# Performance work log

Hardware: AMD Instinct MI355X
Metric: run time of the kernel (lower is better)

Reference implementation:

```python
import jax, jax.numpy as jnp
import numpy as np

ALPHA = 0.5    # SpikeAct surrogate width (act_fun(alpha=0.5))
DECAY = 0.2    # membrane decay
THRESH = 0.5   # firing threshold (requires_grad=False -> constant)


@jax.custom_vjp
def spike_act(x):
    # Heaviside spike with rectangular surrogate gradient
    return (x > 0).astype(x.dtype)

def _sa_fwd(x):
    return spike_act(x), x

def _sa_bwd(x, g):
    return (g * (jnp.abs(x) < ALPHA).astype(g.dtype),)

spike_act.defvjp(_sa_fwd, _sa_bwd)


@jax.custom_vjp
def ei_act(x):
    # EI sign gate with straight-through gradient
    return jnp.sign(x)

def _ei_fwd(x):
    return ei_act(x), None

def _ei_bwd(_, g):
    return (g,)

ei_act.defvjp(_ei_fwd, _ei_bwd)


def conv2d(x, w, b):
    # x: [B,C,H,W], w: [O,I,kh,kw] (OIHW), SAME padding, stride 1
    y = jax.lax.conv_general_dilated(
        x, w, window_strides=(1, 1), padding='SAME',
        dimension_numbers=('NCHW', 'OIHW', 'NCHW'))
    return y + b[None, :, None, None]


def setup_inputs() -> dict:
    key = jax.random.key(0)
    k0, k1, k2 = jax.random.split(key, 3)
    T, B, C, H, W, K = 8, 16, 128, 32, 32, 5
    fan_in = C * K * K
    x = jax.random.normal(k0, (T, B, C, H, W), jnp.float32)
    back_w = jax.random.normal(k1, (C, C, K, K), jnp.float32) / np.float32(np.sqrt(fan_in))
    back_b = jnp.zeros((C,), jnp.float32)
    ei_w = jax.random.normal(k2, (C, C, K, K), jnp.float32) / np.float32(np.sqrt(fan_in))
    ei_b = jnp.zeros((C,), jnp.float32)
    return {"x": x, "back_w": back_w, "back_b": back_b, "ei_w": ei_w, "ei_b": ei_b}


def reference(x, back_w, back_b, ei_w, ei_b):
    # x: [T,B,C,H,W] -> spikes over time [T,B,C,H,W]
    state_shape = x.shape[1:]
    mem0 = jnp.zeros(state_shape, x.dtype)
    spike0 = jnp.zeros(state_shape, x.dtype)

    def step(carry, xt):
        mem, spike = carry
        # integral: decayed mem + feedback-conv sigmoid gate * input
        mem = DECAY * mem + jax.nn.sigmoid(conv2d(spike, back_w, back_b)) * xt
        # calc_spike (if_ei=True path)
        ei_gate = ei_act(conv2d(mem, ei_w, ei_b))
        s = spike_act(mem - THRESH)
        mem = mem * (1.0 - s)
        spike = ei_gate * s
        return (mem, spike), spike

    _, spikes = jax.lax.scan(step, (mem0, spike0), x)
    return spikes
```

## Files before the change

### kernel.cpp

```cpp
#include <hip/hip_runtime.h>
#include <math.h>

#define TDIM 512
#define CCH  128
#define HW   32
#define OCT  4
#define ICT  2
#define NPH  16
#define SW   36
#define TROWS 12
#define PLANE (TROWS * SW)

template<int EPI>
__global__ __launch_bounds__(TDIM, 8) void lif_conv(
    const float* __restrict__ cin,
    const float* __restrict__ wgt,
    const float* __restrict__ bias,
    const float* __restrict__ aux0,
    const float* __restrict__ aux1,
    float* __restrict__ out0,
    float* __restrict__ out1,
    int first)
{
    const int ocg  = blockIdx.x;
    const int half = blockIdx.y;
    const int b    = blockIdx.z;
    const int oc0  = ocg * OCT;
    const int tid  = threadIdx.x;
    const int w    = tid >> 6;
    const int lane = tid & 63;
    const int ks   = w >> 1;
    const int rg   = w & 1;
    const int r0   = half * 16 + rg * 8;
    const int rl   = lane >> 3;
    const int cl   = (lane & 7) * 4;

    const int sks = __builtin_amdgcn_readfirstlane(ks);

    __shared__ __align__(16) float s_in[8 * ICT * PLANE];
    float* tin = s_in + w * (ICT * PLANE);

    float acc[OCT][4];
#pragma unroll
    for (int oc = 0; oc < OCT; ++oc)
#pragma unroll
        for (int j = 0; j < 4; ++j) acc[oc][j] = 0.f;

    if (!(EPI == 0 && first)) {
        const int icbase = ks * 32;
        const int sicb   = sks * 32;
        for (int i = lane; i < ICT * PLANE; i += 64) tin[i] = 0.f;

        for (int ph = 0; ph < NPH; ++ph) {
#pragma unroll
            for (int i = 0; i < 3; ++i) {
                int idx  = i * 64 + lane;
                int p    = (idx >= 96) ? 1 : 0;
                int rem  = idx - p * 96;
                int srow = rem >> 3;
                int sg   = rem & 7;
                int gr   = r0 + srow - 2;
                if ((unsigned)gr < 32u) {
                    float4 v = *(const float4*)&cin[(((size_t)b * CCH + icbase + ph * ICT + p) * HW + gr) * HW + sg * 4];
                    float* dst = &tin[p * PLANE + srow * SW + 2 + sg * 4];
                    *(float2*)dst       = make_float2(v.x, v.y);
                    *(float2*)(dst + 2) = make_float2(v.z, v.w);
                }
            }
#pragma unroll
            for (int ici = 0; ici < ICT; ++ici) {
                float win5[5][8];
#pragma unroll
                for (int kh = 0; kh < 5; ++kh) {
                    const float* src = &tin[ici * PLANE + (rl + kh) * SW + cl];
                    float4 a = *(const float4*)src;
                    float4 c = *(const float4*)(src + 4);
                    win5[kh][0] = a.x; win5[kh][1] = a.y; win5[kh][2] = a.z; win5[kh][3] = a.w;
                    win5[kh][4] = c.x; win5[kh][5] = c.y; win5[kh][6] = c.z; win5[kh][7] = c.w;
                }
                const float* wb = wgt + ((size_t)oc0 * CCH + sicb + ph * ICT + ici) * 25;
#pragma unroll
                for (int oc = 0; oc < OCT; ++oc) {
                    const float* wo = wb + oc * (CCH * 25);
#pragma unroll
                    for (int kh = 0; kh < 5; ++kh) {
#pragma unroll
                        for (int kw = 0; kw < 5; ++kw) {
                            float wv = wo[kh * 5 + kw];
                            acc[oc][0] += win5[kh][kw]     * wv;
                            acc[oc][1] += win5[kh][kw + 1] * wv;
                            acc[oc][2] += win5[kh][kw + 2] * wv;
                            acc[oc][3] += win5[kh][kw + 3] * wv;
                        }
                    }
                }
            }
        }

        __syncthreads();
        float* red = s_in;
        if (ks > 0) {
            const int slot = ((ks - 1) * 128 + rg * 64 + lane) * 17;
#pragma unroll
            for (int oc = 0; oc < OCT; ++oc)
#pragma unroll
                for (int j = 0; j < 4; ++j)
                    red[slot + oc * 4 + j] = acc[oc][j];
        }
        __syncthreads();
        if (ks == 0) {
#pragma unroll
            for (int q = 0; q < 3; ++q) {
                const int slot = (q * 128 + rg * 64 + lane) * 17;
#pragma unroll
                for (int oc = 0; oc < OCT; ++oc)
#pragma unroll
                    for (int j = 0; j < 4; ++j)
                        acc[oc][j] += red[slot + oc * 4 + j];
            }
        }
    }

    if (ks == 0) {
#pragma unroll
        for (int oc = 0; oc < OCT; ++oc) {
            const size_t pidx = (((size_t)b * CCH + oc0 + oc) * HW + (r0 + rl)) * HW + cl;
            const float bia = bias[oc0 + oc];
            float y[4];
#pragma unroll
            for (int j = 0; j < 4; ++j) y[j] = acc[oc][j] + bia;
            if (EPI == 0) {
                float4 xv = *(const float4*)(aux1 + pidx);
                float4 mv;
                if (first) { mv.x = mv.y = mv.z = mv.w = 0.f; }
                else       mv = *(const float4*)(aux0 + pidx);
                float4 mp;
                mp.x = 0.2f * mv.x + (1.f / (1.f + expf(-y[0]))) * xv.x;
                mp.y = 0.2f * mv.y + (1.f / (1.f + expf(-y[1]))) * xv.y;
                mp.z = 0.2f * mv.z + (1.f / (1.f + expf(-y[2]))) * xv.z;
                mp.w = 0.2f * mv.w + (1.f / (1.f + expf(-y[3]))) * xv.w;
                *(float4*)(out0 + pidx) = mp;
            } else {
                float4 m4 = *(const float4*)(aux0 + pidx);
                float g[4] = {
                    (y[0] > 0.f) ? 1.f : ((y[0] < 0.f) ? -1.f : 0.f),
                    (y[1] > 0.f) ? 1.f : ((y[1] < 0.f) ? -1.f : 0.f),
                    (y[2] > 0.f) ? 1.f : ((y[2] < 0.f) ? -1.f : 0.f),
                    (y[3] > 0.f) ? 1.f : ((y[3] < 0.f) ? -1.f : 0.f)};
                float m[4] = {m4.x, m4.y, m4.z, m4.w};
                float4 mn, sp;
                float s0 = (m[0] > 0.5f) ? 1.f : 0.f;
                float s1 = (m[1] > 0.5f) ? 1.f : 0.f;
                float s2 = (m[2] > 0.5f) ? 1.f : 0.f;
                float s3 = (m[3] > 0.5f) ? 1.f : 0.f;
                mn.x = m[0] * (1.f - s0); sp.x = g[0] * s0;
                mn.y = m[1] * (1.f - s1); sp.y = g[1] * s1;
                mn.z = m[2] * (1.f - s2); sp.z = g[2] * s2;
                mn.w = m[3] * (1.f - s3); sp.w = g[3] * s3;
                *(float4*)(out0 + pidx) = mn;
                *(float4*)(out1 + pidx) = sp;
            }
        }
    }
}

extern "C" void kernel_launch(void* const* d_in, const int* in_sizes, int n_in,
                              void* d_out, int out_size, void* d_ws, size_t ws_size,
                              hipStream_t stream) {
    const float* x      = (const float*)d_in[0];
    const float* back_w = (const float*)d_in[1];
    const float* back_b = (const float*)d_in[2];
    const float* ei_w   = (const float*)d_in[3];
    const float* ei_b   = (const float*)d_in[4];
    float* out = (float*)d_out;

    const size_t N = (size_t)16 * CCH * HW * HW;
    float* mem_cur  = (float*)d_ws;
    float* mem_post = mem_cur + N;

    dim3 grid(CCH / OCT, 2, 16);

    for (int t = 0; t < 8; ++t) {
        const float* spike_prev = (t == 0) ? x : (out + (size_t)(t - 1) * N);
        lif_conv<0><<<grid, TDIM, 0, stream>>>(
            spike_prev, back_w, back_b,
            mem_cur, x + (size_t)t * N,
            mem_post, nullptr, (t == 0) ? 1 : 0);
        lif_conv<1><<<grid, TDIM, 0, stream>>>(
            mem_post, ei_w, ei_b,
            mem_post, nullptr,
            mem_cur, out + (size_t)t * N, 0);
    }
}
```

Measured before the change: 2.461 ms.

## Compute 8 pixels per thread with full-image blocks to raise register reuse

```diff
diff --git a/kernel.cpp b/kernel.cpp
--- a/kernel.cpp
+++ b/kernel.cpp
@@ -8,11 +8,11 @@
 #define ICT  2
 #define NPH  16
 #define SW   36
-#define TROWS 12
+#define TROWS 20
 #define PLANE (TROWS * SW)
 
 template<int EPI>
-__global__ __launch_bounds__(TDIM, 8) void lif_conv(
+__global__ __launch_bounds__(TDIM, 2) void lif_conv(
     const float* __restrict__ cin,
     const float* __restrict__ wgt,
     const float* __restrict__ bias,
@@ -23,28 +23,27 @@
     int first)
 {
     const int ocg  = blockIdx.x;
-    const int half = blockIdx.y;
-    const int b    = blockIdx.z;
+    const int b    = blockIdx.y;
     const int oc0  = ocg * OCT;
     const int tid  = threadIdx.x;
     const int w    = tid >> 6;
     const int lane = tid & 63;
     const int ks   = w >> 1;
     const int rg   = w & 1;
-    const int r0   = half * 16 + rg * 8;
-    const int rl   = lane >> 3;
-    const int cl   = (lane & 7) * 4;
+    const int r0   = rg * 16;
+    const int rl   = lane >> 2;
+    const int cl   = (lane & 3) * 8;
 
     const int sks = __builtin_amdgcn_readfirstlane(ks);
 
     __shared__ __align__(16) float s_in[8 * ICT * PLANE];
     float* tin = s_in + w * (ICT * PLANE);
 
-    float acc[OCT][4];
+    float acc[OCT][8];
 #pragma unroll
     for (int oc = 0; oc < OCT; ++oc)
 #pragma unroll
-        for (int j = 0; j < 4; ++j) acc[oc][j] = 0.f;
+        for (int j = 0; j < 8; ++j) acc[oc][j] = 0.f;
 
     if (!(EPI == 0 && first)) {
         const int icbase = ks * 32;
@@ -53,10 +52,10 @@
 
         for (int ph = 0; ph < NPH; ++ph) {
 #pragma unroll
-            for (int i = 0; i < 3; ++i) {
+            for (int i = 0; i < 5; ++i) {
                 int idx  = i * 64 + lane;
-                int p    = (idx >= 96) ? 1 : 0;
-                int rem  = idx - p * 96;
+                int p    = (idx >= 160) ? 1 : 0;
+                int rem  = idx - p * 160;
                 int srow = rem >> 3;
                 int sg   = rem & 7;
                 int gr   = r0 + srow - 2;
@@ -69,28 +68,24 @@
             }
 #pragma unroll
             for (int ici = 0; ici < ICT; ++ici) {
-                float win5[5][8];
+                const float* wb = wgt + ((size_t)oc0 * CCH + sicb + ph * ICT + ici) * 25;
 #pragma unroll
                 for (int kh = 0; kh < 5; ++kh) {
                     const float* src = &tin[ici * PLANE + (rl + kh) * SW + cl];
-                    float4 a = *(const float4*)src;
-                    float4 c = *(const float4*)(src + 4);
-                    win5[kh][0] = a.x; win5[kh][1] = a.y; win5[kh][2] = a.z; win5[kh][3] = a.w;
-                    win5[kh][4] = c.x; win5[kh][5] = c.y; win5[kh][6] = c.z; win5[kh][7] = c.w;
-                }
-                const float* wb = wgt + ((size_t)oc0 * CCH + sicb + ph * ICT + ici) * 25;
-#pragma unroll
-                for (int oc = 0; oc < OCT; ++oc) {
-                    const float* wo = wb + oc * (CCH * 25);
-#pragma unroll
-                    for (int kh = 0; kh < 5; ++kh) {
+                    float4 a  = *(const float4*)src;
+                    float4 c2 = *(const float4*)(src + 4);
+                    float4 e  = *(const float4*)(src + 8);
+                    float wn[12] = {a.x, a.y, a.z, a.w, c2.x, c2.y, c2.z, c2.w,
+                                    e.x, e.y, e.z, e.w};
+#pragma unroll
+                    for (int oc = 0; oc < OCT; ++oc) {
+                        const float* wo = wb + oc * (CCH * 25) + kh * 5;
 #pragma unroll
                         for (int kw = 0; kw < 5; ++kw) {
-                            float wv = wo[kh * 5 + kw];
-                            acc[oc][0] += win5[kh][kw]     * wv;
-                            acc[oc][1] += win5[kh][kw + 1] * wv;
-                            acc[oc][2] += win5[kh][kw + 2] * wv;
-                            acc[oc][3] += win5[kh][kw + 3] * wv;
+                            float wv = wo[kw];
+#pragma unroll
+                            for (int px = 0; px < 8; ++px)
+                                acc[oc][px] += wn[px + kw] * wv;
                         }
                     }
                 }
@@ -99,25 +94,41 @@
 
         __syncthreads();
         float* red = s_in;
-        if (ks > 0) {
-            const int slot = ((ks - 1) * 128 + rg * 64 + lane) * 17;
-#pragma unroll
-            for (int oc = 0; oc < OCT; ++oc)
-#pragma unroll
-                for (int j = 0; j < 4; ++j)
-                    red[slot + oc * 4 + j] = acc[oc][j];
+        if (ks == 1 || ks == 2) {
+            const int slot = ((ks - 1) * 128 + rg * 64 + lane) * 34;
+#pragma unroll
+            for (int oc = 0; oc < OCT; ++oc)
+#pragma unroll
+                for (int j = 0; j < 8; ++j)
+                    red[slot + oc * 8 + j] = acc[oc][j];
         }
         __syncthreads();
         if (ks == 0) {
-#pragma unroll
-            for (int q = 0; q < 3; ++q) {
-                const int slot = (q * 128 + rg * 64 + lane) * 17;
-#pragma unroll
-                for (int oc = 0; oc < OCT; ++oc)
-#pragma unroll
-                    for (int j = 0; j < 4; ++j)
-                        acc[oc][j] += red[slot + oc * 4 + j];
-            }
+            const int s1 = (rg * 64 + lane) * 34;
+            const int s2 = (128 + rg * 64 + lane) * 34;
+#pragma unroll
+            for (int oc = 0; oc < OCT; ++oc)
+#pragma unroll
+                for (int j = 0; j < 8; ++j)
+                    acc[oc][j] += red[s1 + oc * 8 + j] + red[s2 + oc * 8 + j];
+        }
+        __syncthreads();
+        if (ks == 3) {
+            const int slot = (rg * 64 + lane) * 34;
+#pragma unroll
+            for (int oc = 0; oc < OCT; ++oc)
+#pragma unroll
+                for (int j = 0; j < 8; ++j)
+                    red[slot + oc * 8 + j] = acc[oc][j];
+        }
+        __syncthreads();
+        if (ks == 0) {
+            const int slot = (rg * 64 + lane) * 34;
+#pragma unroll
+            for (int oc = 0; oc < OCT; ++oc)
+#pragma unroll
+                for (int j = 0; j < 8; ++j)
+                    acc[oc][j] += red[slot + oc * 8 + j];
         }
     }
 
@@ -126,39 +137,42 @@
         for (int oc = 0; oc < OCT; ++oc) {
             const size_t pidx = (((size_t)b * CCH + oc0 + oc) * HW + (r0 + rl)) * HW + cl;
             const float bia = bias[oc0 + oc];
-            float y[4];
-#pragma unroll
-            for (int j = 0; j < 4; ++j) y[j] = acc[oc][j] + bia;
+            float y[8];
+#pragma unroll
+            for (int j = 0; j < 8; ++j) y[j] = acc[oc][j] + bia;
             if (EPI == 0) {
-                float4 xv = *(const float4*)(aux1 + pidx);
-                float4 mv;
-                if (first) { mv.x = mv.y = mv.z = mv.w = 0.f; }
-                else       mv = *(const float4*)(aux0 + pidx);
-                float4 mp;
-                mp.x = 0.2f * mv.x + (1.f / (1.f + expf(-y[0]))) * xv.x;
-                mp.y = 0.2f * mv.y + (1.f / (1.f + expf(-y[1]))) * xv.y;
-                mp.z = 0.2f * mv.z + (1.f / (1.f + expf(-y[2]))) * xv.z;
-                mp.w = 0.2f * mv.w + (1.f / (1.f + expf(-y[3]))) * xv.w;
-                *(float4*)(out0 + pidx) = mp;
+                float4 xv0 = *(const float4*)(aux1 + pidx);
+                float4 xv1 = *(const float4*)(aux1 + pidx + 4);
+                float xv[8] = {xv0.x, xv0.y, xv0.z, xv0.w, xv1.x, xv1.y, xv1.z, xv1.w};
+                float mv[8] = {0.f, 0.f, 0.f, 0.f, 0.f, 0.f, 0.f, 0.f};
+                if (!first) {
+                    float4 m0 = *(const float4*)(aux0 + pidx);
+                    float4 m1 = *(const float4*)(aux0 + pidx + 4);
+                    mv[0] = m0.x; mv[1] = m0.y; mv[2] = m0.z; mv[3] = m0.w;
+                    mv[4] = m1.x; mv[5] = m1.y; mv[6] = m1.z; mv[7] = m1.w;
+                }
+                float mp[8];
+#pragma unroll
+                for (int j = 0; j < 8; ++j)
+                    mp[j] = 0.2f * mv[j] + (1.f / (1.f + expf(-y[j]))) * xv[j];
+                *(float4*)(out0 + pidx)     = make_float4(mp[0], mp[1], mp[2], mp[3]);
+                *(float4*)(out0 + pidx + 4) = make_float4(mp[4], mp[5], mp[6], mp[7]);
             } else {
-                float4 m4 = *(const float4*)(aux0 + pidx);
-                float g[4] = {
-                    (y[0] > 0.f) ? 1.f : ((y[0] < 0.f) ? -1.f : 0.f),
-                    (y[1] > 0.f) ? 1.f : ((y[1] < 0.f) ? -1.f : 0.f),
-                    (y[2] > 0.f) ? 1.f : ((y[2] < 0.f) ? -1.f : 0.f),
-                    (y[3] > 0.f) ? 1.f : ((y[3] < 0.f) ? -1.f : 0.f)};
-                float m[4] = {m4.x, m4.y, m4.z, m4.w};
-                float4 mn, sp;
-                float s0 = (m[0] > 0.5f) ? 1.f : 0.f;
-                float s1 = (m[1] > 0.5f) ? 1.f : 0.f;
-                float s2 = (m[2] > 0.5f) ? 1.f : 0.f;
-                float s3 = (m[3] > 0.5f) ? 1.f : 0.f;
-                mn.x = m[0] * (1.f - s0); sp.x = g[0] * s0;
-                mn.y = m[1] * (1.f - s1); sp.y = g[1] * s1;
-                mn.z = m[2] * (1.f - s2); sp.z = g[2] * s2;
-                mn.w = m[3] * (1.f - s3); sp.w = g[3] * s3;
-                *(float4*)(out0 + pidx) = mn;
-                *(float4*)(out1 + pidx) = sp;
+                float4 m0 = *(const float4*)(aux0 + pidx);
+                float4 m1 = *(const float4*)(aux0 + pidx + 4);
+                float m[8] = {m0.x, m0.y, m0.z, m0.w, m1.x, m1.y, m1.z, m1.w};
+                float mn[8], sp[8];
+#pragma unroll
+                for (int j = 0; j < 8; ++j) {
+                    float g = (y[j] > 0.f) ? 1.f : ((y[j] < 0.f) ? -1.f : 0.f);
+                    float s = (m[j] > 0.5f) ? 1.f : 0.f;
+                    mn[j] = m[j] * (1.f - s);
+                    sp[j] = g * s;
+                }
+                *(float4*)(out0 + pidx)     = make_float4(mn[0], mn[1], mn[2], mn[3]);
+                *(float4*)(out0 + pidx + 4) = make_float4(mn[4], mn[5], mn[6], mn[7]);
+                *(float4*)(out1 + pidx)     = make_float4(sp[0], sp[1], sp[2], sp[3]);
+                *(float4*)(out1 + pidx + 4) = make_float4(sp[4], sp[5], sp[6], sp[7]);
             }
         }
     }
@@ -178,7 +192,7 @@
     float* mem_cur  = (float*)d_ws;
     float* mem_post = mem_cur + N;
 
-    dim3 grid(CCH / OCT, 2, 16);
+    dim3 grid(CCH / OCT, 16);
 
     for (int t = 0; t < 8; ++t) {
         const float* spike_prev = (t == 0) ? x : (out + (size_t)(t - 1) * N);
```

New measurement: 2.336 ms. 5.1% less time.
